# Kernel tuning notes

Measured on AMD Instinct MI355X. Metric: run time of the kernel, lower is better.

Reference implementation:

```python
import jax, jax.numpy as jnp
import numpy as np

N = 50000          # nodes
DEG = 16           # graph_max_neighbor
E = N * DEG        # edges (sorted by receiver)
DIM = 128          # config.hidden_dimension
EDGE_DIM = 32
EPS = 1e-5


def _ln(x, scale, offset, mask):
    # masked LayerNorm over last axis: normalize per row, then apply node mask
    m = jnp.mean(x, axis=-1, keepdims=True)
    v = jnp.mean(jnp.square(x - m), axis=-1, keepdims=True)
    return ((x - m) * jax.lax.rsqrt(v + EPS) * scale + offset) * mask


def setup_inputs() -> dict:
    key = jax.random.key(0)
    ks = jax.random.split(key, 12)
    node_inp = jax.random.normal(ks[0], (N, DIM), jnp.float32)
    edge_feat = jax.random.normal(ks[1], (E, EDGE_DIM), jnp.float32)
    node_mask = jnp.ones((N, 1), jnp.float32)
    senders = jax.random.randint(ks[2], (E,), 0, N, jnp.int32)
    receivers = jnp.repeat(jnp.arange(N, dtype=jnp.int32), DEG)  # sorted, DEG per node
    din_e = 2 * DIM + EDGE_DIM
    s = lambda d: 1.0 / np.sqrt(d)
    We1 = jax.random.normal(ks[3], (din_e, 2 * DIM), jnp.float32) * s(din_e)
    be1 = jnp.zeros((2 * DIM,), jnp.float32)
    We2 = jax.random.normal(ks[4], (2 * DIM, DIM), jnp.float32) * s(2 * DIM)
    be2 = jnp.zeros((DIM,), jnp.float32)
    g_msg = jnp.ones((DIM,), jnp.float32)
    b_msg = jnp.zeros((DIM,), jnp.float32)
    Wn1 = jax.random.normal(ks[5], (2 * DIM, 2 * DIM), jnp.float32) * s(2 * DIM)
    bn1 = jnp.zeros((2 * DIM,), jnp.float32)
    Wn2 = jax.random.normal(ks[6], (2 * DIM, DIM), jnp.float32) * s(2 * DIM)
    bn2 = jnp.zeros((DIM,), jnp.float32)
    g_node = jnp.ones((DIM,), jnp.float32)
    b_node = jnp.zeros((DIM,), jnp.float32)
    return dict(node_inp=node_inp, edge_feat=edge_feat, node_mask=node_mask,
                We1=We1, be1=be1, We2=We2, be2=be2, g_msg=g_msg, b_msg=b_msg,
                Wn1=Wn1, bn1=bn1, Wn2=Wn2, bn2=bn2, g_node=g_node, b_node=b_node,
                senders=senders, receivers=receivers)


def reference(node_inp, edge_feat, node_mask, We1, be1, We2, be2, g_msg, b_msg,
              Wn1, bn1, Wn2, bn2, g_node, b_node, senders, receivers):
    # gather + concat -> edge MLP (swish, no final activation; haiku MLP default)
    msg_input = jnp.concatenate(
        [node_inp[senders], node_inp[receivers], edge_feat], axis=-1)  # [E, 2*DIM+EDGE_DIM]
    h = jax.nn.swish(msg_input @ We1 + be1)
    messages = h @ We2 + be2                                           # [E, DIM]
    # scatter-reduce to receivers (sorted), mean over max neighbors
    agg = jax.ops.segment_sum(messages, receivers, num_segments=node_inp.shape[0],
                              indices_are_sorted=True) / DEG
    agg = _ln(agg, g_msg, b_msg, node_mask)
    # node update MLP + residual + masked LN
    nf = jnp.concatenate([node_inp, agg], axis=-1)                     # [N, 2*DIM]
    nf = jax.nn.swish(nf @ Wn1 + bn1) @ Wn2 + bn2                      # [N, DIM]
    nf = node_inp + nf
    return _ln(nf, g_node, b_node, node_mask)
```

## Files before the change

### kernel.cpp

```cpp
#include <hip/hip_runtime.h>

typedef _Float16 F16;
typedef _Float16 half8 __attribute__((ext_vector_type(8)));
typedef _Float16 half2 __attribute__((ext_vector_type(2)));
typedef float f32x4 __attribute__((ext_vector_type(4)));

#define N_NODES 50000
#define DEG 16
#define N_EDGES (N_NODES * DEG)
#define DIM 128

__device__ __forceinline__ float frcp(float x) { float r; asm("v_rcp_f32 %0, %1" : "=v"(r) : "v"(x)); return r; }
__device__ __forceinline__ float frsq(float x) { float r; asm("v_rsq_f32 %0, %1" : "=v"(r) : "v"(x)); return r; }
__device__ __forceinline__ float fexp2(float x) { float r; asm("v_exp_f32 %0, %1" : "=v"(r) : "v"(x)); return r; }
__device__ __forceinline__ float swishf(float x) { return x * frcp(1.0f + fexp2(x * -1.442695041f)); }

__device__ __forceinline__ half8 cvt8(f32x4 a, f32x4 b) {
    half8 h; h[0]=(F16)a[0]; h[1]=(F16)a[1]; h[2]=(F16)a[2]; h[3]=(F16)a[3];
    h[4]=(F16)b[0]; h[5]=(F16)b[1]; h[6]=(F16)b[2]; h[7]=(F16)b[3]; return h;
}

__device__ __forceinline__ void pack_one(const float* src, F16* dst, int idx,
                                         int K, int NC, int ld, int row0, int split) {
    int j = idx & 7;
    int l = (idx >> 3) & 63;
    int blob = idx >> 9;
    int ntiles = NC >> 4;
    int tcol = blob % ntiles;
    int c = blob / ntiles;
    int k = c * 32 + ((l >> 4) * 8) + j;
    int col = tcol * 16 + (l & 15);
    int sr = row0 + k, sc = col;
    if (split && col >= split) { sr += K; sc -= split; }
    dst[idx] = (F16)src[(size_t)sr * ld + sc];
}

__global__ void k_pack_all(const float* __restrict__ We1, const float* __restrict__ We2,
                           const float* __restrict__ Wn1, const float* __restrict__ Wn2,
                           F16* w1abp, F16* w1ep, F16* we2p, F16* wn1p, F16* wn2p) {
    int b = blockIdx.x, t = threadIdx.x;
    if (b < 256)      pack_one(We1, w1abp, (b - 0)   * 256 + t, 128, 512, 256, 0,   256);
    else if (b < 288) pack_one(We1, w1ep,  (b - 256) * 256 + t, 32,  256, 256, 256, 0);
    else if (b < 416) pack_one(We2, we2p,  (b - 288) * 256 + t, 256, 128, 128, 0,   0);
    else if (b < 672) pack_one(Wn1, wn1p,  (b - 416) * 256 + t, 256, 256, 256, 0,   0);
    else              pack_one(Wn2, wn2p,  (b - 672) * 256 + t, 256, 128, 128, 0,   0);
}

#define PAS 152
__global__ __launch_bounds__(256, 2) void k_proj(
    const float* __restrict__ node_inp, const float* __restrict__ be1,
    const F16* __restrict__ w1abp, F16* __restrict__ Ps, F16* __restrict__ Pr)
{
    __shared__ __align__(16) F16 A[64 * PAS];
    const int t = threadIdx.x;
    const int n0 = blockIdx.x * 64;

    #pragma unroll
    for (int i = 0; i < 4; ++i) {
        int id = t + i * 256; int row = id >> 4, c = id & 15;
        int gn = n0 + row; if (gn >= N_NODES) gn = N_NODES - 1;
        f32x4 v0 = *(const f32x4*)(node_inp + (size_t)gn * DIM + c * 8);
        f32x4 v1 = *(const f32x4*)(node_inp + (size_t)gn * DIM + c * 8 + 4);
        *(half8*)&A[row * PAS + c * 8] = cvt8(v0, v1);
    }
    __syncthreads();

    const int lane = t & 63, wn = t >> 6;
    const int lcol = lane & 15, quad = lane >> 4;

    f32x4 acc[4][8] = {};
    #pragma unroll
    for (int c = 0; c < 4; ++c) {
        half8 af[4];
        #pragma unroll
        for (int rt = 0; rt < 4; ++rt)
            af[rt] = *(const half8*)&A[(rt * 16 + lcol) * PAS + c * 32 + quad * 8];
        const F16* wp = w1abp + (((size_t)(c * 32 + wn * 8)) * 64 + lane) * 8;
        #pragma unroll
        for (int nt = 0; nt < 8; ++nt) {
            half8 bv = *(const half8*)(wp + (size_t)nt * 512);
            #pragma unroll
            for (int rt = 0; rt < 4; ++rt)
                acc[rt][nt] = __builtin_amdgcn_mfma_f32_16x16x32_f16(af[rt], bv, acc[rt][nt], 0, 0, 0);
        }
    }

    F16* dst = (wn < 2) ? Ps : Pr;
    const int cb = (wn & 1) * 128;
    #pragma unroll
    for (int nt = 0; nt < 8; ++nt) {
        int col = cb + nt * 16 + lcol;
        float bias = (wn >= 2) ? be1[col] : 0.0f;
        #pragma unroll
        for (int rt = 0; rt < 4; ++rt) {
            #pragma unroll
            for (int r = 0; r < 4; ++r) {
                int gn = n0 + rt * 16 + quad * 4 + r;
                if (gn < N_NODES) dst[(size_t)gn * 256 + col] = (F16)(acc[rt][nt][r] + bias);
            }
        }
    }
}

#define PGS2 136
__global__ __launch_bounds__(256, 4) void k_edge(
    const F16* __restrict__ Ps, const F16* Pr,
    const float* __restrict__ edge_feat, const int* __restrict__ senders,
    const F16* __restrict__ w1ep, F16* Hm)
{
    __shared__ __align__(16) F16 Pg[4 * 16 * PGS2];
    __shared__ int sidx[64];
    const int t = threadIdx.x;
    const int n0 = blockIdx.x * 4;
    const int e0 = n0 * 16;
    const int lane = t & 63, nd = t >> 6;
    const int lcol = lane & 15, quad = lane >> 4;
    const int n = n0 + nd;

    if (t < 64) sidx[t] = senders[e0 + t];

    f32x4 v0 = *(const f32x4*)(edge_feat + (size_t)(e0 + nd * 16 + lcol) * 32 + quad * 8);
    f32x4 v1 = *(const f32x4*)(edge_feat + (size_t)(e0 + nd * 16 + lcol) * 32 + quad * 8 + 4);
    half8 a = cvt8(v0, v1);
    __syncthreads();

    F16* pg = &Pg[nd * 16 * PGS2];
    #pragma unroll
    for (int h = 0; h < 2; ++h) {
        #pragma unroll
        for (int i = 0; i < 4; ++i) {
            int id = lane + i * 64; int row = id >> 4, c = id & 15;
            int s = sidx[nd * 16 + row];
            half8 ps = *(const half8*)(Ps + (size_t)s * 256 + h * 128 + c * 8);
            half8 pr = *(const half8*)(Pr + (size_t)n * 256 + h * 128 + c * 8);
            *(half8*)&pg[row * PGS2 + c * 8] = ps + pr;
        }
        f32x4 acc[8] = {};
        #pragma unroll
        for (int j = 0; j < 8; ++j) {
            half8 bv = *(const half8*)(w1ep + (((size_t)(h * 8 + j)) * 64 + lane) * 8);
            acc[j] = __builtin_amdgcn_mfma_f32_16x16x32_f16(a, bv, acc[j], 0, 0, 0);
        }
        #pragma unroll
        for (int j = 0; j < 8; ++j) {
            const F16* pgp = &pg[(quad * 4) * PGS2 + j * 16 + lcol];
            float s = 0.f;
            #pragma unroll
            for (int r = 0; r < 4; ++r) {
                float x = acc[j][r] + (float)pgp[r * PGS2];
                s += swishf(x);
            }
            s += __shfl_xor(s, 16, 64);
            s += __shfl_xor(s, 32, 64);
            if (lane < 16) Hm[(size_t)n * 256 + h * 128 + j * 16 + lane] = (F16)(s * 0.0625f);
        }
    }
}

#define XS 280
#define FSS 139
__global__ __launch_bounds__(256, 4) void k_node(
    const float* __restrict__ node_inp, const F16* Hm,
    const float* __restrict__ be2, const float* __restrict__ g_msg, const float* __restrict__ b_msg,
    const float* __restrict__ bn1, const float* __restrict__ bn2,
    const float* __restrict__ g_node, const float* __restrict__ b_node,
    const float* __restrict__ node_mask,
    const F16* __restrict__ we2p, const F16* __restrict__ wn1p, const F16* __restrict__ wn2p,
    float* out)
{
    __shared__ __align__(16) unsigned char smem[64 * XS * 2];
    F16* X = (F16*)smem;
    float* Fs = (float*)smem;

    const int t = threadIdx.x;
    const int n0 = blockIdx.x * 64;
    const int lane = t & 63, w = t >> 6;
    const int lcol = lane & 15, quad = lane >> 4;

    #pragma unroll
    for (int i = 0; i < 4; ++i) {
        int id = t + i * 256; int row = id >> 4, c = id & 15;
        int gn = n0 + row; if (gn >= N_NODES) gn = N_NODES - 1;
        f32x4 v0 = *(const f32x4*)(node_inp + (size_t)gn * DIM + c * 8);
        f32x4 v1 = *(const f32x4*)(node_inp + (size_t)gn * DIM + c * 8 + 4);
        *(half8*)&X[row * XS + c * 8] = cvt8(v0, v1);
    }

    {
        const int r0 = w * 16;
        int gr = n0 + r0 + lcol; if (gr >= N_NODES) gr = N_NODES - 1;
        const F16* hrow = Hm + (size_t)gr * 256;
        f32x4 acc[8] = {};
        #pragma unroll
        for (int c = 0; c < 8; ++c) {
            half8 af = *(const half8*)(hrow + c * 32 + quad * 8);
            const F16* wp = we2p + (((size_t)(c * 8)) * 64 + lane) * 8;
            #pragma unroll
            for (int nt = 0; nt < 8; ++nt) {
                half8 bv = *(const half8*)(wp + (size_t)nt * 512);
                acc[nt] = __builtin_amdgcn_mfma_f32_16x16x32_f16(af, bv, acc[nt], 0, 0, 0);
            }
        }
        #pragma unroll
        for (int nt = 0; nt < 8; ++nt) {
            int col = nt * 16 + lcol;
            float b = be2[col];
            #pragma unroll
            for (int r = 0; r < 4; ++r)
                X[(r0 + quad * 4 + r) * XS + 128 + col] = (F16)(acc[nt][r] + b);
        }
    }
    __syncthreads();

    {
        int row = t >> 2, q = t & 3;
        int gn = n0 + row; if (gn >= N_NODES) gn = N_NODES - 1;
        float vv[32]; float sum = 0.f, sq = 0.f;
        #pragma unroll
        for (int j = 0; j < 4; ++j) {
            half8 hv = *(const half8*)&X[row * XS + 128 + q * 32 + j * 8];
            #pragma unroll
            for (int k = 0; k < 8; ++k) { float f = (float)hv[k]; vv[j*8+k] = f; sum += f; sq += f*f; }
        }
        sum += __shfl_xor(sum, 1, 64); sq += __shfl_xor(sq, 1, 64);
        sum += __shfl_xor(sum, 2, 64); sq += __shfl_xor(sq, 2, 64);
        float mean = sum * (1.0f / DIM);
        float rs = frsq(sq * (1.0f / DIM) - mean * mean + 1e-5f);
        float msk = node_mask[gn];
        #pragma unroll
        for (int j = 0; j < 16; ++j) {
            int col = q * 32 + j * 2;
            half2 o;
            o[0] = (F16)(((vv[j*2]   - mean) * rs * g_msg[col]   + b_msg[col])   * msk);
            o[1] = (F16)(((vv[j*2+1] - mean) * rs * g_msg[col+1] + b_msg[col+1]) * msk);
            *(half2*)&X[row * XS + 128 + col] = o;
        }
    }
    __syncthreads();

    {
        f32x4 acc1[4][4] = {};
        #pragma unroll
        for (int c = 0; c < 8; ++c) {
            half8 af[4];
            #pragma unroll
            for (int rt = 0; rt < 4; ++rt)
                af[rt] = *(const half8*)&X[(rt * 16 + lcol) * XS + c * 32 + quad * 8];
            const F16* wp = wn1p + (((size_t)(c * 16 + w * 4)) * 64 + lane) * 8;
            #pragma unroll
            for (int nt = 0; nt < 4; ++nt) {
                half8 bv = *(const half8*)(wp + (size_t)nt * 512);
                #pragma unroll
                for (int rt = 0; rt < 4; ++rt)
                    acc1[rt][nt] = __builtin_amdgcn_mfma_f32_16x16x32_f16(af[rt], bv, acc1[rt][nt], 0, 0, 0);
            }
        }
        __syncthreads();
        #pragma unroll
        for (int nt = 0; nt < 4; ++nt) {
            int col = w * 64 + nt * 16 + lcol;
            float b = bn1[col];
            #pragma unroll
            for (int rt = 0; rt < 4; ++rt)
                #pragma unroll
                for (int r = 0; r < 4; ++r) {
                    float x = acc1[rt][nt][r] + b;
                    X[(rt * 16 + quad * 4 + r) * XS + col] = (F16)swishf(x);
                }
        }
    }
    __syncthreads();

    {
        f32x4 acc2[4][2] = {};
        #pragma unroll
        for (int c = 0; c < 8; ++c) {
            half8 af[4];
            #pragma unroll
            for (int rt = 0; rt < 4; ++rt)
                af[rt] = *(const half8*)&X[(rt * 16 + lcol) * XS + c * 32 + quad * 8];
            const F16* wp = wn2p + (((size_t)(c * 8 + w * 2)) * 64 + lane) * 8;
            #pragma unroll
            for (int nt = 0; nt < 2; ++nt) {
                half8 bv = *(const half8*)(wp + (size_t)nt * 512);
                #pragma unroll
                for (int rt = 0; rt < 4; ++rt)
                    acc2[rt][nt] = __builtin_amdgcn_mfma_f32_16x16x32_f16(af[rt], bv, acc2[rt][nt], 0, 0, 0);
            }
        }
        __syncthreads();
        #pragma unroll
        for (int nt = 0; nt < 2; ++nt) {
            int col = w * 32 + nt * 16 + lcol;
            float b = bn2[col];
            #pragma unroll
            for (int rt = 0; rt < 4; ++rt)
                #pragma unroll
                for (int r = 0; r < 4; ++r)
                    Fs[(rt * 16 + quad * 4 + r) * FSS + col] = acc2[rt][nt][r] + b;
        }
    }
    __syncthreads();

    {
        int row = t >> 2, q = t & 3;
        int gn = n0 + row;
        f32x4 xr[8];
        float sum = 0.f, sq = 0.f;
        if (gn < N_NODES) {
            #pragma unroll
            for (int j = 0; j < 8; ++j) {
                f32x4 aa = *(const f32x4*)&Fs[row * FSS + q * 32 + j * 4];
                f32x4 ni = *(const f32x4*)(node_inp + (size_t)gn * DIM + q * 32 + j * 4);
                f32x4 x = aa + ni;
                xr[j] = x;
                sum += x[0] + x[1] + x[2] + x[3];
                sq  += x[0]*x[0] + x[1]*x[1] + x[2]*x[2] + x[3]*x[3];
            }
        }
        sum += __shfl_xor(sum, 1, 64); sq += __shfl_xor(sq, 1, 64);
        sum += __shfl_xor(sum, 2, 64); sq += __shfl_xor(sq, 2, 64);
        if (gn < N_NODES) {
            float mean = sum * (1.0f / DIM);
            float rs = frsq(sq * (1.0f / DIM) - mean * mean + 1e-5f);
            float msk = node_mask[gn];
            #pragma unroll
            for (int j = 0; j < 8; ++j) {
                f32x4 o;
                #pragma unroll
                for (int qq = 0; qq < 4; ++qq) {
                    int col = q * 32 + j * 4 + qq;
                    o[qq] = ((xr[j][qq] - mean) * rs * g_node[col] + b_node[col]) * msk;
                }
                *(f32x4*)(out + (size_t)gn * DIM + q * 32 + j * 4) = o;
            }
        }
    }
}


extern "C" void kernel_launch(void* const* d_in, const int* in_sizes, int n_in,
                              void* d_out, int out_size, void* d_ws, size_t ws_size,
                              hipStream_t stream)
{
    const float* node_inp  = (const float*)d_in[0];
    const float* edge_feat = (const float*)d_in[1];
    const float* node_mask = (const float*)d_in[2];
    const float* We1 = (const float*)d_in[3];
    const float* be1 = (const float*)d_in[4];
    const float* We2 = (const float*)d_in[5];
    const float* be2 = (const float*)d_in[6];
    const float* g_msg = (const float*)d_in[7];
    const float* b_msg = (const float*)d_in[8];
    const float* Wn1 = (const float*)d_in[9];
    const float* bn1 = (const float*)d_in[10];
    const float* Wn2 = (const float*)d_in[11];
    const float* bn2 = (const float*)d_in[12];
    const float* g_node = (const float*)d_in[13];
    const float* b_node = (const float*)d_in[14];
    const int* senders = (const int*)d_in[15];
    float* out = (float*)d_out;

    char* ws = (char*)d_ws;
    F16* Ps = (F16*)ws;
    size_t off = (size_t)N_NODES * 256 * 2;
    F16* w1abp = (F16*)(ws + off); off += 128 * 512 * 2;
    F16* w1ep  = (F16*)(ws + off); off += 32 * 256 * 2;
    F16* we2p  = (F16*)(ws + off); off += 256 * 128 * 2;
    F16* wn1p  = (F16*)(ws + off); off += 256 * 256 * 2;
    F16* wn2p  = (F16*)(ws + off); off += 256 * 128 * 2;

    F16* PrHm = (F16*)d_out;

    k_pack_all<<<dim3(800), dim3(256), 0, stream>>>(We1, We2, Wn1, Wn2,
                                                    w1abp, w1ep, we2p, wn1p, wn2p);

    k_proj<<<dim3((N_NODES + 63) / 64), dim3(256), 0, stream>>>(node_inp, be1, w1abp, Ps, PrHm);

    k_edge<<<dim3(N_NODES / 4), dim3(256), 0, stream>>>(Ps, PrHm, edge_feat, senders, w1ep, PrHm);

    k_node<<<dim3((N_NODES + 63) / 64), dim3(256), 0, stream>>>(
        node_inp, PrHm, be2, g_msg, b_msg, bn1, bn2, g_node, b_node, node_mask,
        we2p, wn1p, wn2p, out);
}
```

Measured before the change: 362.8 us.

## Reorder projection layout so edge kernel gathers directly into MFMA accumulators

k_proj now writes Ps/Pr in a permuted column layout, so each lane of k_edge can load its 16 accumulator values as contiguous half8 vectors. It also splits the accumulation into two passes to allow higher occupancy. k_edge drops the shared-memory staging and barrier: it reads sender indices and projections into registers and seeds the MFMA accumulators with Ps+Pr. k_node stages Hm through shared memory in two K halves and splits the output columns across waves, in place of per-wave rows reading Hm from global memory. The Hm column order stays the same, but the Ps/Pr layout coupling across kernels is fragile.

```diff
diff --git a/kernel.cpp b/kernel.cpp
--- a/kernel.cpp
+++ b/kernel.cpp
@@ -2,6 +2,7 @@
 
 typedef _Float16 F16;
 typedef _Float16 half8 __attribute__((ext_vector_type(8)));
+typedef _Float16 half4 __attribute__((ext_vector_type(4)));
 typedef _Float16 half2 __attribute__((ext_vector_type(2)));
 typedef float f32x4 __attribute__((ext_vector_type(4)));
 
@@ -47,7 +48,7 @@
 }
 
 #define PAS 152
-__global__ __launch_bounds__(256, 2) void k_proj(
+__global__ __launch_bounds__(256, 4) void k_proj(
     const float* __restrict__ node_inp, const float* __restrict__ be1,
     const F16* __restrict__ w1abp, F16* __restrict__ Ps, F16* __restrict__ Pr)
 {
@@ -65,77 +66,88 @@
     }
     __syncthreads();
 
-    const int lane = t & 63, wn = t >> 6;
+    const int lane = t & 63, w = t >> 6;
     const int lcol = lane & 15, quad = lane >> 4;
 
-    f32x4 acc[4][8] = {};
-    #pragma unroll
-    for (int c = 0; c < 4; ++c) {
-        half8 af[4];
+    F16* dst = (w < 2) ? Ps : Pr;
+    const int cb = (w & 1) * 128;
+
+    #pragma unroll
+    for (int p = 0; p < 2; ++p) {
+        f32x4 acc[4][4] = {};
+        #pragma unroll
+        for (int c = 0; c < 4; ++c) {
+            half8 af[4];
+            #pragma unroll
+            for (int rt = 0; rt < 4; ++rt)
+                af[rt] = *(const half8*)&A[(rt * 16 + lcol) * PAS + c * 32 + quad * 8];
+            const F16* wp = w1abp + (((size_t)(c * 32 + w * 8 + p * 4)) * 64 + lane) * 8;
+            #pragma unroll
+            for (int nt = 0; nt < 4; ++nt) {
+                half8 bv = *(const half8*)(wp + (size_t)nt * 512);
+                #pragma unroll
+                for (int rt = 0; rt < 4; ++rt)
+                    acc[rt][nt] = __builtin_amdgcn_mfma_f32_16x16x32_f16(af[rt], bv, acc[rt][nt], 0, 0, 0);
+            }
+        }
+        float bias[4];
+        #pragma unroll
+        for (int nt = 0; nt < 4; ++nt)
+            bias[nt] = (w >= 2) ? be1[cb + p * 64 + nt * 16 + lcol] : 0.0f;
         #pragma unroll
         for (int rt = 0; rt < 4; ++rt)
-            af[rt] = *(const half8*)&A[(rt * 16 + lcol) * PAS + c * 32 + quad * 8];
-        const F16* wp = w1abp + (((size_t)(c * 32 + wn * 8)) * 64 + lane) * 8;
-        #pragma unroll
-        for (int nt = 0; nt < 8; ++nt) {
-            half8 bv = *(const half8*)(wp + (size_t)nt * 512);
-            #pragma unroll
-            for (int rt = 0; rt < 4; ++rt)
-                acc[rt][nt] = __builtin_amdgcn_mfma_f32_16x16x32_f16(af[rt], bv, acc[rt][nt], 0, 0, 0);
-        }
-    }
-
-    F16* dst = (wn < 2) ? Ps : Pr;
-    const int cb = (wn & 1) * 128;
-    #pragma unroll
-    for (int nt = 0; nt < 8; ++nt) {
-        int col = cb + nt * 16 + lcol;
-        float bias = (wn >= 2) ? be1[col] : 0.0f;
-        #pragma unroll
-        for (int rt = 0; rt < 4; ++rt) {
             #pragma unroll
             for (int r = 0; r < 4; ++r) {
                 int gn = n0 + rt * 16 + quad * 4 + r;
-                if (gn < N_NODES) dst[(size_t)gn * 256 + col] = (F16)(acc[rt][nt][r] + bias);
-            }
-        }
-    }
-}
-
-#define PGS2 136
+                half4 o;
+                #pragma unroll
+                for (int nt = 0; nt < 4; ++nt) o[nt] = (F16)(acc[rt][nt][r] + bias[nt]);
+                if (gn < N_NODES)
+                    *(half4*)(dst + (size_t)gn * 256 + lcol * 16 + (w & 1) * 8 + p * 4) = o;
+            }
+    }
+}
+
 __global__ __launch_bounds__(256, 4) void k_edge(
     const F16* __restrict__ Ps, const F16* Pr,
     const float* __restrict__ edge_feat, const int* __restrict__ senders,
     const F16* __restrict__ w1ep, F16* Hm)
 {
-    __shared__ __align__(16) F16 Pg[4 * 16 * PGS2];
-    __shared__ int sidx[64];
     const int t = threadIdx.x;
-    const int n0 = blockIdx.x * 4;
-    const int e0 = n0 * 16;
     const int lane = t & 63, nd = t >> 6;
+    const int n = blockIdx.x * 4 + nd;
+    const int e0 = n * 16;
     const int lcol = lane & 15, quad = lane >> 4;
-    const int n = n0 + nd;
-
-    if (t < 64) sidx[t] = senders[e0 + t];
-
-    f32x4 v0 = *(const f32x4*)(edge_feat + (size_t)(e0 + nd * 16 + lcol) * 32 + quad * 8);
-    f32x4 v1 = *(const f32x4*)(edge_feat + (size_t)(e0 + nd * 16 + lcol) * 32 + quad * 8 + 4);
+
+    int srow[4];
+    #pragma unroll
+    for (int r = 0; r < 4; ++r) srow[r] = senders[e0 + quad * 4 + r];
+
+    f32x4 v0 = *(const f32x4*)(edge_feat + (size_t)(e0 + lcol) * 32 + quad * 8);
+    f32x4 v1 = *(const f32x4*)(edge_feat + (size_t)(e0 + lcol) * 32 + quad * 8 + 4);
     half8 a = cvt8(v0, v1);
-    __syncthreads();
-
-    F16* pg = &Pg[nd * 16 * PGS2];
+
+    half8 pr0 = *(const half8*)(Pr + (size_t)n * 256 + lcol * 16);
+    half8 pr1 = *(const half8*)(Pr + (size_t)n * 256 + lcol * 16 + 8);
+    half8 ps0[4], ps1[4];
+    #pragma unroll
+    for (int r = 0; r < 4; ++r) {
+        const F16* p = Ps + (size_t)srow[r] * 256 + lcol * 16;
+        ps0[r] = *(const half8*)p;
+        ps1[r] = *(const half8*)(p + 8);
+    }
+    float prf[16];
+    #pragma unroll
+    for (int j = 0; j < 8; ++j) { prf[j] = (float)pr0[j]; prf[8 + j] = (float)pr1[j]; }
+
     #pragma unroll
     for (int h = 0; h < 2; ++h) {
-        #pragma unroll
-        for (int i = 0; i < 4; ++i) {
-            int id = lane + i * 64; int row = id >> 4, c = id & 15;
-            int s = sidx[nd * 16 + row];
-            half8 ps = *(const half8*)(Ps + (size_t)s * 256 + h * 128 + c * 8);
-            half8 pr = *(const half8*)(Pr + (size_t)n * 256 + h * 128 + c * 8);
-            *(half8*)&pg[row * PGS2 + c * 8] = ps + pr;
-        }
-        f32x4 acc[8] = {};
+        f32x4 acc[8];
+        #pragma unroll
+        for (int j = 0; j < 8; ++j)
+            #pragma unroll
+            for (int r = 0; r < 4; ++r)
+                acc[j][r] = (float)((h ? ps1 : ps0)[r][j]) + prf[h * 8 + j];
         #pragma unroll
         for (int j = 0; j < 8; ++j) {
             half8 bv = *(const half8*)(w1ep + (((size_t)(h * 8 + j)) * 64 + lane) * 8);
@@ -143,16 +155,10 @@
         }
         #pragma unroll
         for (int j = 0; j < 8; ++j) {
-            const F16* pgp = &pg[(quad * 4) * PGS2 + j * 16 + lcol];
-            float s = 0.f;
-            #pragma unroll
-            for (int r = 0; r < 4; ++r) {
-                float x = acc[j][r] + (float)pgp[r * PGS2];
-                s += swishf(x);
-            }
+            float s = swishf(acc[j][0]) + swishf(acc[j][1]) + swishf(acc[j][2]) + swishf(acc[j][3]);
             s += __shfl_xor(s, 16, 64);
             s += __shfl_xor(s, 32, 64);
-            if (lane < 16) Hm[(size_t)n * 256 + h * 128 + j * 16 + lane] = (F16)(s * 0.0625f);
+            if (lane < 16) Hm[(size_t)n * 256 + (h * 8 + j) * 16 + lane] = (F16)(s * 0.0625f);
         }
     }
 }
@@ -177,38 +183,50 @@
     const int lane = t & 63, w = t >> 6;
     const int lcol = lane & 15, quad = lane >> 4;
 
-    #pragma unroll
-    for (int i = 0; i < 4; ++i) {
-        int id = t + i * 256; int row = id >> 4, c = id & 15;
-        int gn = n0 + row; if (gn >= N_NODES) gn = N_NODES - 1;
-        f32x4 v0 = *(const f32x4*)(node_inp + (size_t)gn * DIM + c * 8);
-        f32x4 v1 = *(const f32x4*)(node_inp + (size_t)gn * DIM + c * 8 + 4);
-        *(half8*)&X[row * XS + c * 8] = cvt8(v0, v1);
-    }
-
-    {
-        const int r0 = w * 16;
-        int gr = n0 + r0 + lcol; if (gr >= N_NODES) gr = N_NODES - 1;
-        const F16* hrow = Hm + (size_t)gr * 256;
-        f32x4 acc[8] = {};
-        #pragma unroll
-        for (int c = 0; c < 8; ++c) {
-            half8 af = *(const half8*)(hrow + c * 32 + quad * 8);
-            const F16* wp = we2p + (((size_t)(c * 8)) * 64 + lane) * 8;
-            #pragma unroll
-            for (int nt = 0; nt < 8; ++nt) {
+    f32x4 accm[4][2] = {};
+
+    #pragma unroll
+    for (int kh = 0; kh < 2; ++kh) {
+        #pragma unroll
+        for (int i = 0; i < 4; ++i) {
+            int id = t + i * 256; int row = id >> 4, c = id & 15;
+            int gn = n0 + row; if (gn >= N_NODES) gn = N_NODES - 1;
+            *(half8*)&X[row * XS + 128 + c * 8] =
+                *(const half8*)(Hm + (size_t)gn * 256 + kh * 128 + c * 8);
+            if (kh == 0) {
+                f32x4 u0 = *(const f32x4*)(node_inp + (size_t)gn * DIM + c * 8);
+                f32x4 u1 = *(const f32x4*)(node_inp + (size_t)gn * DIM + c * 8 + 4);
+                *(half8*)&X[row * XS + c * 8] = cvt8(u0, u1);
+            }
+        }
+        __syncthreads();
+        #pragma unroll
+        for (int c = 0; c < 4; ++c) {
+            half8 af[4];
+            #pragma unroll
+            for (int rt = 0; rt < 4; ++rt)
+                af[rt] = *(const half8*)&X[(rt * 16 + lcol) * XS + 128 + c * 32 + quad * 8];
+            const F16* wp = we2p + (((size_t)((kh * 4 + c) * 8 + w * 2)) * 64 + lane) * 8;
+            #pragma unroll
+            for (int nt = 0; nt < 2; ++nt) {
                 half8 bv = *(const half8*)(wp + (size_t)nt * 512);
-                acc[nt] = __builtin_amdgcn_mfma_f32_16x16x32_f16(af, bv, acc[nt], 0, 0, 0);
-            }
-        }
-        #pragma unroll
-        for (int nt = 0; nt < 8; ++nt) {
-            int col = nt * 16 + lcol;
-            float b = be2[col];
+                #pragma unroll
+                for (int rt = 0; rt < 4; ++rt)
+                    accm[rt][nt] = __builtin_amdgcn_mfma_f32_16x16x32_f16(af[rt], bv, accm[rt][nt], 0, 0, 0);
+            }
+        }
+        __syncthreads();
+    }
+
+    #pragma unroll
+    for (int nt = 0; nt < 2; ++nt) {
+        int col = w * 32 + nt * 16 + lcol;
+        float b = be2[col];
+        #pragma unroll
+        for (int rt = 0; rt < 4; ++rt)
             #pragma unroll
             for (int r = 0; r < 4; ++r)
-                X[(r0 + quad * 4 + r) * XS + 128 + col] = (F16)(acc[nt][r] + b);
-        }
+                X[(rt * 16 + quad * 4 + r) * XS + 128 + col] = (F16)(accm[rt][nt][r] + b);
     }
     __syncthreads();
 
```

New measurement: 382.0 us. 5.3% more time.
